# Kernel optimization log

Measured on AMD Instinct MI355X. Metric: run time of the kernel, lower is better.

Reference implementation:

```python
import jax, jax.numpy as jnp
import numpy as np

NODE_NUM = 100000
LAYER_NUM = 4
EMB = 128
FEAT = 256
BATCH = 4096
NEIGH = 32
EPS = 1e-12  # F.normalize default eps


def setup_inputs() -> dict:
    key = jax.random.key(0)
    ks = jax.random.split(key, 10)
    std = 1.0 / np.sqrt(EMB)
    return {
        "layers": jax.random.randint(ks[0], (BATCH,), 0, LAYER_NUM),
        "node_i": jax.random.randint(ks[1], (BATCH,), 0, NODE_NUM),
        "neighs_i": jax.random.randint(ks[2], (BATCH, LAYER_NUM, NEIGH), 0, NODE_NUM),
        "features": jax.random.normal(ks[3], (NODE_NUM, FEAT), dtype=jnp.float32),
        "layer_embs": jax.random.uniform(ks[4], (NODE_NUM, LAYER_NUM, EMB), dtype=jnp.float32, minval=-1.0, maxval=1.0),
        "neigh_emb_trans": jax.random.normal(ks[5], (LAYER_NUM, FEAT, EMB), dtype=jnp.float32) * std,
        "trans_weights": jax.random.normal(ks[6], (EMB, EMB), dtype=jnp.float32) * std,
        "trans_weights_s1": jax.random.normal(ks[7], (EMB, EMB), dtype=jnp.float32) * std,
        "trans_weights_s2": jax.random.normal(ks[8], (EMB, 1), dtype=jnp.float32) * std,
    }


def reference(layers, node_i, neighs_i, features, layer_embs, neigh_emb_trans,
              trans_weights, trans_weights_s1, trans_weights_s2):
    # Gather neighbor features: [B, L, J, F]
    feats_n = features[neighs_i]
    # Per-layer linear transform == diagonal of torch's 'bijk,akm->bijam' over (i,a):
    # [B, L, J, M]
    h = jnp.einsum('bljf,lfm->bljm', feats_n, neigh_emb_trans)
    # Sum over neighbors -> [B, L, M]
    h = h.sum(axis=2)
    # Attention over layers: tanh(h @ Ws1) @ Ws2 -> [B, L]
    scores = jnp.squeeze(jnp.tanh(h @ trans_weights_s1) @ trans_weights_s2, axis=-1)
    att = jax.nn.softmax(scores, axis=1)  # [B, L]
    # Attention-weighted layer aggregation -> [B, M]
    agg = jnp.einsum('bl,blm->bm', att, h)
    node_embed = agg @ trans_weights  # [B, M]
    final = node_embed + layer_embs[node_i, layers]  # residual with per-(node,layer) emb
    # F.normalize(dim=1): x / max(||x||_2, eps)
    norm = jnp.linalg.norm(final, axis=1, keepdims=True)
    return final / jnp.maximum(norm, EPS)
```

## Files before the change

### kernel.cpp

```cpp
#include <hip/hip_runtime.h>
#include <hip/hip_bf16.h>
#include <math.h>

#define BATCH 4096
#define LNUM  4
#define NEIGH 32
#define FEAT  256
#define EMB   128

__global__ __launch_bounds__(256) void k1_gather_sum(
    const int* __restrict__ neighs, const float* __restrict__ features,
    float* __restrict__ S) {
  int b = blockIdx.x;
  int l = threadIdx.x >> 6;
  int lane = threadIdx.x & 63;
  const int* nbr = neighs + ((size_t)b * LNUM + l) * NEIGH;
  int myn = (lane < NEIGH) ? nbr[lane] : 0;
  float4 acc = make_float4(0.f, 0.f, 0.f, 0.f);
#pragma unroll 8
  for (int j = 0; j < NEIGH; ++j) {
    int n = __shfl(myn, j, 64);
    float4 v = ((const float4*)(features + (size_t)n * FEAT))[lane];
    acc.x += v.x; acc.y += v.y; acc.z += v.z; acc.w += v.w;
  }
  ((float4*)S)[((size_t)b * LNUM + l) * (FEAT / 4) + lane] = acc;
}

__global__ __launch_bounds__(128) void k2_h(
    const float* __restrict__ S, const float* __restrict__ W,
    float* __restrict__ H) {
  __shared__ float sS[32 * FEAT];
  int l = blockIdx.y;
  int b0 = blockIdx.x * 32;
  const float* Wl = W + (size_t)l * FEAT * EMB;
  for (int i = threadIdx.x; i < 32 * (FEAT / 4); i += 128) {
    int r = i >> 6;
    int c = i & 63;
    ((float4*)sS)[i] =
        ((const float4*)S)[((size_t)(b0 + r) * LNUM + l) * (FEAT / 4) + c];
  }
  __syncthreads();
  int tx = threadIdx.x & 31;
  int ty = threadIdx.x >> 5;
  float acc[8][4] = {};
#pragma unroll 4
  for (int k = 0; k < FEAT; ++k) {
    float4 w = ((const float4*)(Wl + (size_t)k * EMB))[tx];
#pragma unroll
    for (int r = 0; r < 8; ++r) {
      float s = sS[(ty * 8 + r) * FEAT + k];
      acc[r][0] += s * w.x; acc[r][1] += s * w.y;
      acc[r][2] += s * w.z; acc[r][3] += s * w.w;
    }
  }
#pragma unroll
  for (int r = 0; r < 8; ++r) {
    int b = b0 + ty * 8 + r;
    float4 o = make_float4(acc[r][0], acc[r][1], acc[r][2], acc[r][3]);
    ((float4*)H)[((size_t)b * LNUM + l) * (EMB / 4) + tx] = o;
  }
}

__global__ __launch_bounds__(128) void k3_scores(
    const float* __restrict__ H, const float* __restrict__ Ws1,
    const float* __restrict__ Ws2, float* __restrict__ scores) {
  __shared__ float sH[32 * EMB];
  int r0 = blockIdx.x * 32;
  for (int i = threadIdx.x; i < 32 * (EMB / 4); i += 128) {
    ((float4*)sH)[i] = ((const float4*)H)[(size_t)r0 * (EMB / 4) + i];
  }
  __syncthreads();
  int tx = threadIdx.x & 31;
  int ty = threadIdx.x >> 5;
  float acc[8][4] = {};
#pragma unroll 4
  for (int k = 0; k < EMB; ++k) {
    float4 w = ((const float4*)(Ws1 + (size_t)k * EMB))[tx];
#pragma unroll
    for (int r = 0; r < 8; ++r) {
      float h = sH[(ty * 8 + r) * EMB + k];
      acc[r][0] += h * w.x; acc[r][1] += h * w.y;
      acc[r][2] += h * w.z; acc[r][3] += h * w.w;
    }
  }
  float4 w2 = ((const float4*)Ws2)[tx];
#pragma unroll
  for (int r = 0; r < 8; ++r) {
    float p = tanhf(acc[r][0]) * w2.x + tanhf(acc[r][1]) * w2.y +
              tanhf(acc[r][2]) * w2.z + tanhf(acc[r][3]) * w2.w;
#pragma unroll
    for (int m = 1; m < 32; m <<= 1) p += __shfl_xor(p, m, 64);
    if (tx == 0) scores[r0 + ty * 8 + r] = p;
  }
}

__global__ __launch_bounds__(256) void k4_out(
    const float* __restrict__ H, const float* __restrict__ scores,
    const float* __restrict__ Wt, const int* __restrict__ node_i,
    const int* __restrict__ layers, const float* __restrict__ layer_embs,
    float* __restrict__ out) {
  __shared__ float sAgg[16 * EMB];
  __shared__ float sAtt[16 * LNUM];
  int b0 = blockIdx.x * 16;
  int tid = threadIdx.x;
  if (tid < 16 * LNUM) {
    int b = b0 + (tid >> 2);
    int l = tid & 3;
    float s0 = scores[b * 4 + 0], s1 = scores[b * 4 + 1];
    float s2 = scores[b * 4 + 2], s3 = scores[b * 4 + 3];
    float mx = fmaxf(fmaxf(s0, s1), fmaxf(s2, s3));
    float sum = expf(s0 - mx) + expf(s1 - mx) + expf(s2 - mx) + expf(s3 - mx);
    sAtt[tid] = expf(scores[b * 4 + l] - mx) / sum;
  }
  __syncthreads();
  for (int i = tid; i < 16 * EMB; i += 256) {
    int r = i >> 7;
    int m = i & 127;
    int b = b0 + r;
    float a = 0.f;
#pragma unroll
    for (int l = 0; l < LNUM; ++l)
      a += sAtt[r * 4 + l] * H[((size_t)b * LNUM + l) * EMB + m];
    sAgg[i] = a;
  }
  __syncthreads();
  int tx = tid & 31;
  int ty = tid >> 5;
  float acc[2][4] = {};
#pragma unroll 4
  for (int k = 0; k < EMB; ++k) {
    float4 w = ((const float4*)(Wt + (size_t)k * EMB))[tx];
#pragma unroll
    for (int r = 0; r < 2; ++r) {
      float a = sAgg[(ty * 2 + r) * EMB + k];
      acc[r][0] += a * w.x; acc[r][1] += a * w.y;
      acc[r][2] += a * w.z; acc[r][3] += a * w.w;
    }
  }
#pragma unroll
  for (int r = 0; r < 2; ++r) {
    int b = b0 + ty * 2 + r;
    int node = node_i[b];
    int lay = layers[b];
    float4 e =
        ((const float4*)(layer_embs + ((size_t)node * LNUM + lay) * EMB))[tx];
    acc[r][0] += e.x; acc[r][1] += e.y; acc[r][2] += e.z; acc[r][3] += e.w;
    float ss = acc[r][0] * acc[r][0] + acc[r][1] * acc[r][1] +
               acc[r][2] * acc[r][2] + acc[r][3] * acc[r][3];
#pragma unroll
    for (int m = 1; m < 32; m <<= 1) ss += __shfl_xor(ss, m, 64);
    float inv = 1.0f / fmaxf(sqrtf(ss), 1e-12f);
    float4 o = make_float4(acc[r][0] * inv, acc[r][1] * inv, acc[r][2] * inv,
                           acc[r][3] * inv);
    ((float4*)out)[(size_t)b * (EMB / 4) + tx] = o;
  }
}

extern "C" void kernel_launch(void* const* d_in, const int* in_sizes, int n_in,
                              void* d_out, int out_size, void* d_ws,
                              size_t ws_size, hipStream_t stream) {
  const int* layers = (const int*)d_in[0];
  const int* node_i = (const int*)d_in[1];
  const int* neighs = (const int*)d_in[2];
  const float* features = (const float*)d_in[3];
  const float* layer_embs = (const float*)d_in[4];
  const float* neigh_emb_trans = (const float*)d_in[5];
  const float* trans_weights = (const float*)d_in[6];
  const float* trans_weights_s1 = (const float*)d_in[7];
  const float* trans_weights_s2 = (const float*)d_in[8];
  float* out = (float*)d_out;

  float* S = (float*)d_ws;
  float* H = S + (size_t)BATCH * LNUM * FEAT;
  float* scores = H + (size_t)BATCH * LNUM * EMB;

  k1_gather_sum<<<dim3(BATCH), 256, 0, stream>>>(neighs, features, S);
  k2_h<<<dim3(BATCH / 32, LNUM), 128, 0, stream>>>(S, neigh_emb_trans, H);
  k3_scores<<<dim3(BATCH * LNUM / 32), 128, 0, stream>>>(
      H, trans_weights_s1, trans_weights_s2, scores);
  k4_out<<<dim3(BATCH / 16), 256, 0, stream>>>(H, scores, trans_weights,
                                               node_i, layers, layer_embs, out);
}
```

Measured before the change: 441.1 us.

## Fuse gather, layer transform, attention and output into one kernel

Replaces the four kernels with a single kernel. Each block handles 8 batch rows: it gathers and sums the neighbor features into shared memory, then applies the per-layer transform, the attention scores, the softmax aggregation and the output projection with normalization, all from shared memory. This removes the global round trips of S, H and scores and three launch boundaries. In exchange there are only 512 blocks, each using about 48KB of LDS, and weights are reread per block with smaller tiles, which may limit occupancy and the latency hiding for the gather.

```diff
diff --git a/kernel.cpp b/kernel.cpp
--- a/kernel.cpp
+++ b/kernel.cpp
@@ -8,151 +8,131 @@
 #define FEAT  256
 #define EMB   128
 
-__global__ __launch_bounds__(256) void k1_gather_sum(
+#define B_TILE 8
+#define ROWS   (B_TILE * LNUM)
+
+__global__ __launch_bounds__(256) void fused_liamne(
+    const int* __restrict__ layers, const int* __restrict__ node_i,
     const int* __restrict__ neighs, const float* __restrict__ features,
-    float* __restrict__ S) {
-  int b = blockIdx.x;
-  int l = threadIdx.x >> 6;
-  int lane = threadIdx.x & 63;
-  const int* nbr = neighs + ((size_t)b * LNUM + l) * NEIGH;
-  int myn = (lane < NEIGH) ? nbr[lane] : 0;
-  float4 acc = make_float4(0.f, 0.f, 0.f, 0.f);
+    const float* __restrict__ layer_embs, const float* __restrict__ W,
+    const float* __restrict__ Wt, const float* __restrict__ Ws1,
+    const float* __restrict__ Ws2, float* __restrict__ out) {
+  __shared__ float sS[ROWS][FEAT];
+  __shared__ float sH[ROWS][EMB];
+  __shared__ float sc[ROWS];
+
+  int b0 = blockIdx.x * B_TILE;
+  int tid = threadIdx.x;
+  int w = tid >> 6;
+  int lane = tid & 63;
+
+#pragma unroll
+  for (int i = 0; i < 8; ++i) {
+    int r = w * 8 + i;
+    int lb = r >> 2, l = r & 3;
+    const int* nbr = neighs + ((size_t)(b0 + lb) * LNUM + l) * NEIGH;
+    int myn = nbr[lane & 31];
+    float ax = 0.f, ay = 0.f, az = 0.f, aw = 0.f;
 #pragma unroll 8
-  for (int j = 0; j < NEIGH; ++j) {
-    int n = __shfl(myn, j, 64);
-    float4 v = ((const float4*)(features + (size_t)n * FEAT))[lane];
-    acc.x += v.x; acc.y += v.y; acc.z += v.z; acc.w += v.w;
-  }
-  ((float4*)S)[((size_t)b * LNUM + l) * (FEAT / 4) + lane] = acc;
-}
-
-__global__ __launch_bounds__(128) void k2_h(
-    const float* __restrict__ S, const float* __restrict__ W,
-    float* __restrict__ H) {
-  __shared__ float sS[32 * FEAT];
-  int l = blockIdx.y;
-  int b0 = blockIdx.x * 32;
-  const float* Wl = W + (size_t)l * FEAT * EMB;
-  for (int i = threadIdx.x; i < 32 * (FEAT / 4); i += 128) {
-    int r = i >> 6;
-    int c = i & 63;
-    ((float4*)sS)[i] =
-        ((const float4*)S)[((size_t)(b0 + r) * LNUM + l) * (FEAT / 4) + c];
+    for (int j = 0; j < NEIGH; ++j) {
+      int n = __shfl(myn, j, 64);
+      float4 v = ((const float4*)(features + (size_t)n * FEAT))[lane];
+      ax += v.x; ay += v.y; az += v.z; aw += v.w;
+    }
+    ((float4*)sS[r])[lane] = make_float4(ax, ay, az, aw);
   }
   __syncthreads();
-  int tx = threadIdx.x & 31;
-  int ty = threadIdx.x >> 5;
-  float acc[8][4] = {};
-#pragma unroll 4
-  for (int k = 0; k < FEAT; ++k) {
-    float4 w = ((const float4*)(Wl + (size_t)k * EMB))[tx];
+
+  {
+    const float* Wl = W + (size_t)w * FEAT * EMB;
+    float acc[8][2] = {};
+    for (int k = 0; k < FEAT; k += 4) {
+      float4 s[8];
 #pragma unroll
-    for (int r = 0; r < 8; ++r) {
-      float s = sS[(ty * 8 + r) * FEAT + k];
-      acc[r][0] += s * w.x; acc[r][1] += s * w.y;
-      acc[r][2] += s * w.z; acc[r][3] += s * w.w;
+      for (int lb = 0; lb < 8; ++lb)
+        s[lb] = *(const float4*)&sS[lb * 4 + w][k];
+#pragma unroll
+      for (int kk = 0; kk < 4; ++kk) {
+        float2 wv = *(const float2*)&Wl[(size_t)(k + kk) * EMB + lane * 2];
+#pragma unroll
+        for (int lb = 0; lb < 8; ++lb) {
+          float sv = ((const float*)&s[lb])[kk];
+          acc[lb][0] += sv * wv.x;
+          acc[lb][1] += sv * wv.y;
+        }
+      }
+    }
+#pragma unroll
+    for (int lb = 0; lb < 8; ++lb)
+      *(float2*)&sH[lb * 4 + w][lane * 2] = make_float2(acc[lb][0], acc[lb][1]);
+  }
+  __syncthreads();
+
+  {
+    float acc[8][2] = {};
+    for (int k = 0; k < EMB; k += 4) {
+      float4 h[8];
+#pragma unroll
+      for (int i = 0; i < 8; ++i)
+        h[i] = *(const float4*)&sH[w * 8 + i][k];
+#pragma unroll
+      for (int kk = 0; kk < 4; ++kk) {
+        float2 wv = *(const float2*)&Ws1[(size_t)(k + kk) * EMB + lane * 2];
+#pragma unroll
+        for (int i = 0; i < 8; ++i) {
+          float hv = ((const float*)&h[i])[kk];
+          acc[i][0] += hv * wv.x;
+          acc[i][1] += hv * wv.y;
+        }
+      }
+    }
+    float2 w2 = *(const float2*)&Ws2[lane * 2];
+#pragma unroll
+    for (int i = 0; i < 8; ++i) {
+      float p = tanhf(acc[i][0]) * w2.x + tanhf(acc[i][1]) * w2.y;
+#pragma unroll
+      for (int m = 1; m < 64; m <<= 1) p += __shfl_xor(p, m, 64);
+      if (lane == 0) sc[w * 8 + i] = p;
     }
   }
-#pragma unroll
-  for (int r = 0; r < 8; ++r) {
-    int b = b0 + ty * 8 + r;
-    float4 o = make_float4(acc[r][0], acc[r][1], acc[r][2], acc[r][3]);
-    ((float4*)H)[((size_t)b * LNUM + l) * (EMB / 4) + tx] = o;
-  }
-}
+  __syncthreads();
 
-__global__ __launch_bounds__(128) void k3_scores(
-    const float* __restrict__ H, const float* __restrict__ Ws1,
-    const float* __restrict__ Ws2, float* __restrict__ scores) {
-  __shared__ float sH[32 * EMB];
-  int r0 = blockIdx.x * 32;
-  for (int i = threadIdx.x; i < 32 * (EMB / 4); i += 128) {
-    ((float4*)sH)[i] = ((const float4*)H)[(size_t)r0 * (EMB / 4) + i];
+  float* sAgg = &sS[0][0];
+  for (int i = tid; i < B_TILE * EMB; i += 256) {
+    int lb = i >> 7, m = i & 127;
+    float s0 = sc[lb * 4 + 0], s1 = sc[lb * 4 + 1];
+    float s2 = sc[lb * 4 + 2], s3 = sc[lb * 4 + 3];
+    float mx = fmaxf(fmaxf(s0, s1), fmaxf(s2, s3));
+    float e0 = expf(s0 - mx), e1 = expf(s1 - mx);
+    float e2 = expf(s2 - mx), e3 = expf(s3 - mx);
+    float inv = 1.0f / (e0 + e1 + e2 + e3);
+    float a = e0 * sH[lb * 4 + 0][m] + e1 * sH[lb * 4 + 1][m] +
+              e2 * sH[lb * 4 + 2][m] + e3 * sH[lb * 4 + 3][m];
+    sAgg[i] = a * inv;
   }
   __syncthreads();
-  int tx = threadIdx.x & 31;
-  int ty = threadIdx.x >> 5;
-  float acc[8][4] = {};
-#pragma unroll 4
-  for (int k = 0; k < EMB; ++k) {
-    float4 w = ((const float4*)(Ws1 + (size_t)k * EMB))[tx];
-#pragma unroll
-    for (int r = 0; r < 8; ++r) {
-      float h = sH[(ty * 8 + r) * EMB + k];
-      acc[r][0] += h * w.x; acc[r][1] += h * w.y;
-      acc[r][2] += h * w.z; acc[r][3] += h * w.w;
+
+  {
+    int g = tid >> 5;
+    int t = tid & 31;
+    float ax = 0.f, ay = 0.f, az = 0.f, aw = 0.f;
+    for (int k = 0; k < EMB; ++k) {
+      float4 wv = ((const float4*)(Wt + (size_t)k * EMB))[t];
+      float a = sAgg[g * EMB + k];
+      ax += a * wv.x; ay += a * wv.y; az += a * wv.z; aw += a * wv.w;
     }
-  }
-  float4 w2 = ((const float4*)Ws2)[tx];
-#pragma unroll
-  for (int r = 0; r < 8; ++r) {
-    float p = tanhf(acc[r][0]) * w2.x + tanhf(acc[r][1]) * w2.y +
-              tanhf(acc[r][2]) * w2.z + tanhf(acc[r][3]) * w2.w;
-#pragma unroll
-    for (int m = 1; m < 32; m <<= 1) p += __shfl_xor(p, m, 64);
-    if (tx == 0) scores[r0 + ty * 8 + r] = p;
-  }
-}
-
-__global__ __launch_bounds__(256) void k4_out(
-    const float* __restrict__ H, const float* __restrict__ scores,
-    const float* __restrict__ Wt, const int* __restrict__ node_i,
-    const int* __restrict__ layers, const float* __restrict__ layer_embs,
-    float* __restrict__ out) {
-  __shared__ float sAgg[16 * EMB];
-  __shared__ float sAtt[16 * LNUM];
-  int b0 = blockIdx.x * 16;
-  int tid = threadIdx.x;
-  if (tid < 16 * LNUM) {
-    int b = b0 + (tid >> 2);
-    int l = tid & 3;
-    float s0 = scores[b * 4 + 0], s1 = scores[b * 4 + 1];
-    float s2 = scores[b * 4 + 2], s3 = scores[b * 4 + 3];
-    float mx = fmaxf(fmaxf(s0, s1), fmaxf(s2, s3));
-    float sum = expf(s0 - mx) + expf(s1 - mx) + expf(s2 - mx) + expf(s3 - mx);
-    sAtt[tid] = expf(scores[b * 4 + l] - mx) / sum;
-  }
-  __syncthreads();
-  for (int i = tid; i < 16 * EMB; i += 256) {
-    int r = i >> 7;
-    int m = i & 127;
-    int b = b0 + r;
-    float a = 0.f;
-#pragma unroll
-    for (int l = 0; l < LNUM; ++l)
-      a += sAtt[r * 4 + l] * H[((size_t)b * LNUM + l) * EMB + m];
-    sAgg[i] = a;
-  }
-  __syncthreads();
-  int tx = tid & 31;
-  int ty = tid >> 5;
-  float acc[2][4] = {};
-#pragma unroll 4
-  for (int k = 0; k < EMB; ++k) {
-    float4 w = ((const float4*)(Wt + (size_t)k * EMB))[tx];
-#pragma unroll
-    for (int r = 0; r < 2; ++r) {
-      float a = sAgg[(ty * 2 + r) * EMB + k];
-      acc[r][0] += a * w.x; acc[r][1] += a * w.y;
-      acc[r][2] += a * w.z; acc[r][3] += a * w.w;
-    }
-  }
-#pragma unroll
-  for (int r = 0; r < 2; ++r) {
-    int b = b0 + ty * 2 + r;
+    int b = b0 + g;
     int node = node_i[b];
     int lay = layers[b];
     float4 e =
-        ((const float4*)(layer_embs + ((size_t)node * LNUM + lay) * EMB))[tx];
-    acc[r][0] += e.x; acc[r][1] += e.y; acc[r][2] += e.z; acc[r][3] += e.w;
-    float ss = acc[r][0] * acc[r][0] + acc[r][1] * acc[r][1] +
-               acc[r][2] * acc[r][2] + acc[r][3] * acc[r][3];
+        ((const float4*)(layer_embs + ((size_t)node * LNUM + lay) * EMB))[t];
+    ax += e.x; ay += e.y; az += e.z; aw += e.w;
+    float ss = ax * ax + ay * ay + az * az + aw * aw;
 #pragma unroll
     for (int m = 1; m < 32; m <<= 1) ss += __shfl_xor(ss, m, 64);
     float inv = 1.0f / fmaxf(sqrtf(ss), 1e-12f);
-    float4 o = make_float4(acc[r][0] * inv, acc[r][1] * inv, acc[r][2] * inv,
-                           acc[r][3] * inv);
-    ((float4*)out)[(size_t)b * (EMB / 4) + tx] = o;
+    ((float4*)(out + (size_t)b * EMB))[t] =
+        make_float4(ax * inv, ay * inv, az * inv, aw * inv);
   }
 }
 
@@ -170,14 +150,7 @@
   const float* trans_weights_s2 = (const float*)d_in[8];
   float* out = (float*)d_out;
 
-  float* S = (float*)d_ws;
-  float* H = S + (size_t)BATCH * LNUM * FEAT;
-  float* scores = H + (size_t)BATCH * LNUM * EMB;
-
-  k1_gather_sum<<<dim3(BATCH), 256, 0, stream>>>(neighs, features, S);
-  k2_h<<<dim3(BATCH / 32, LNUM), 128, 0, stream>>>(S, neigh_emb_trans, H);
-  k3_scores<<<dim3(BATCH * LNUM / 32), 128, 0, stream>>>(
-      H, trans_weights_s1, trans_weights_s2, scores);
-  k4_out<<<dim3(BATCH / 16), 256, 0, stream>>>(H, scores, trans_weights,
-                                               node_i, layers, layer_embs, out);
+  fused_liamne<<<dim3(BATCH / B_TILE), 256, 0, stream>>>(
+      layers, node_i, neighs, features, layer_embs, neigh_emb_trans,
+      trans_weights, trans_weights_s1, trans_weights_s2, out);
 }
```

New measurement: 404.7 us. 1.09x faster.
